# Kernel tuning notes

Measured on AMD Instinct MI355X. Metric: run time of the kernel, lower is better.

Reference implementation:

```python
import jax, jax.numpy as jnp
import numpy as np

QD, KD, HID, NH = 256, 320, 256, 8
NQ, NK, NB = 4096, 4096, 16
DH = HID // NH
EPS = 1e-5
SCALE = float(1.0 / np.sqrt(DH))


def setup_inputs() -> dict:
    key = jax.random.key(0)
    ks = jax.random.split(key, 12)
    s = 0.02
    return {
        "query_nodes": jax.random.normal(ks[0], (NQ, QD), jnp.float32),
        "key_nodes": jax.random.normal(ks[1], (NK, KD), jnp.float32),
        "Wq": jax.random.normal(ks[2], (QD, HID), jnp.float32) * s,
        "bq": jnp.zeros((HID,), jnp.float32),
        "Wk": jax.random.normal(ks[3], (KD, HID), jnp.float32) * s,
        "bk": jnp.zeros((HID,), jnp.float32),
        "Wv": jax.random.normal(ks[4], (KD, HID), jnp.float32) * s,
        "bv": jnp.zeros((HID,), jnp.float32),
        "in_proj_w": jax.random.normal(ks[5], (3 * HID, HID), jnp.float32) * s,
        "in_proj_b": jnp.zeros((3 * HID,), jnp.float32),
        "mha_ow": jax.random.normal(ks[6], (HID, HID), jnp.float32) * s,
        "mha_ob": jnp.zeros((HID,), jnp.float32),
        "Wo": jax.random.normal(ks[7], (HID, QD), jnp.float32) * s,
        "bo": jnp.zeros((QD,), jnp.float32),
        "ln_g": jnp.ones((QD,), jnp.float32),
        "ln_b": jnp.zeros((QD,), jnp.float32),
        "query_batch_idx": jnp.sort(jax.random.randint(ks[8], (NQ,), 0, NB, jnp.int32)),
        "key_batch_idx": jnp.sort(jax.random.randint(ks[9], (NK,), 0, NB, jnp.int32)),
    }


def reference(query_nodes, key_nodes, Wq, bq, Wk, bk, Wv, bv, in_proj_w, in_proj_b,
              mha_ow, mha_ob, Wo, bo, ln_g, ln_b, query_batch_idx, key_batch_idx):
    # outer projections
    q = query_nodes @ Wq + bq          # [NQ, HID]
    k = key_nodes @ Wk + bk            # [NK, HID]
    v = key_nodes @ Wv + bv            # [NK, HID]
    # nn.MultiheadAttention internal in_proj (weights stored [3H, H], applied as x @ W.T)
    q2 = q @ in_proj_w[:HID].T + in_proj_b[:HID]
    k2 = k @ in_proj_w[HID:2 * HID].T + in_proj_b[HID:2 * HID]
    v2 = v @ in_proj_w[2 * HID:].T + in_proj_b[2 * HID:]
    qh = q2.reshape(NQ, NH, DH)
    kh = k2.reshape(NK, NH, DH)
    vh = v2.reshape(NK, NH, DH)
    scores = jnp.einsum('qhd,khd->hqk', qh, kh) * SCALE   # [NH, NQ, NK]
    mask = query_batch_idx[:, None] != key_batch_idx[None, :]  # True = disallowed
    scores = jnp.where(mask[None], -jnp.inf, scores)
    attn = jax.nn.softmax(scores, axis=-1)
    ctx = jnp.einsum('hqk,khd->qhd', attn, vh).reshape(NQ, HID)
    ctx = ctx @ mha_ow + mha_ob        # MHA internal out_proj
    out = ctx @ Wo + bo                # module out_proj back to query_dim
    x = query_nodes + out              # residual (dropout is identity in eval)
    mu = jnp.mean(x, axis=-1, keepdims=True)
    var = jnp.mean((x - mu) ** 2, axis=-1, keepdims=True)
    return (x - mu) / jnp.sqrt(var + EPS) * ln_g + ln_b
```

## Files before the change

kernel.cpp:

```cpp
#include <hip/hip_runtime.h>
#include <hip/hip_bf16.h>
#include <math.h>

#define NQ 4096
#define NK 4096
#define QD 256
#define KD 320
#define HID 256
#define NH 8
#define DH 32
#define NB 16
#define LN_EPS 1e-5f
#define ATT_SCALE 0.17677669529663687f

typedef unsigned short ushort_t;
typedef __attribute__((ext_vector_type(8))) short bf16x8_t;
typedef __attribute__((ext_vector_type(4))) short bf16x4_t;
typedef __attribute__((ext_vector_type(4))) float f32x4_t;

#define OFF_QNB   0
#define OFF_KNB   524288
#define OFF_Q2B   1179648
#define OFF_K2B   1703936
#define OFF_V2B   2228224
#define OFF_CTXB  2752512
#define OFF_XRES  3276800
#define OFF_WQB   4325376
#define OFF_WKB   4358144
#define OFF_WVB   4399104
#define OFF_WINB  4440064
#define OFF_MOWB  4538368
#define OFF_WOTB  4571136
#define OFF_WQT   4603904
#define OFF_WKT   4636672
#define OFF_WVT   4677632
#define OFF_WOT   4718592
#define OFF_BQ    4751360
#define OFF_BK    4751616
#define OFF_BV    4751872
#define OFF_BINP  4752128
#define OFF_MOB   4752896
#define OFF_BO    4753152
#define OFF_LNG   4753408
#define OFF_LNB   4753664
#define OFF_BEFFQ 4753920
#define OFF_BEFFK 4754176
#define OFF_BEFFV 4754432
#define OFF_BEFFO 4754688
#define OFF_KST   4754944
#define OFF_KEN   4754960
#define OFF_FLAG  4754976

__device__ __forceinline__ float bf16_bits_to_f(ushort_t s) {
    unsigned int u = (unsigned int)s << 16;
    float f;
    __builtin_memcpy(&f, &u, 4);
    return f;
}

__device__ __forceinline__ ushort_t f_to_bf16_bits(float v) {
    __hip_bfloat16 t = (__hip_bfloat16)v;
    ushort_t b;
    __builtin_memcpy(&b, &t, 2);
    return b;
}

__global__ void k_detect(const ushort_t* __restrict__ probe,
                         int* __restrict__ flag) {
    __shared__ float red[4];
    int t = threadIdx.x;
    float mx = 0.f;
    for (int i = t; i < 4096; i += 256) {
        float f = fabsf(bf16_bits_to_f(probe[i]));
        if (!(f == f)) f = 1e38f;
        mx = fmaxf(mx, f);
    }
    for (int off = 32; off; off >>= 1) mx = fmaxf(mx, __shfl_xor(mx, off, 64));
    if ((t & 63) == 0) red[t >> 6] = mx;
    __syncthreads();
    if (t == 0) {
        mx = fmaxf(fmaxf(red[0], red[1]), fmaxf(red[2], red[3]));
        *flag = (mx < 100.f) ? 1 : 0;
    }
}

struct Ptrs16 { const void* p[16]; };

#define CVT_TOTAL 2918912

__global__ void k_cvt_all(Ptrs16 ps, float* __restrict__ ws,
                          const int* __restrict__ flag) {
    const int ns[16]   = {1048576,1310720,65536,256,81920,256,81920,256,
                          196608,768,65536,256,65536,256,256,256};
    const int doff[16] = {OFF_QNB,OFF_KNB,OFF_WQB,OFF_BQ,OFF_WKB,OFF_BK,
                          OFF_WVB,OFF_BV,OFF_WINB,OFF_BINP,OFF_MOWB,
                          OFF_MOB,OFF_WOTB,OFF_BO,OFF_LNG,OFF_LNB};
    const int typ[16]  = {0,0,0,1,0,1,0,1,0,1,0,1,2,1,1,1};
    int gid = blockIdx.x * 256 + threadIdx.x;
    if (gid >= CVT_TOTAL) return;
    int fl = *flag;
    int base = 0;
#pragma unroll
    for (int s = 0; s < 16; ++s) {
        int n = ns[s];
        if (gid < base + n) {
            int i = gid - base;
            if (typ[s] == 1) {
                float v = fl ? bf16_bits_to_f(((const ushort_t*)ps.p[s])[i])
                             : ((const float*)ps.p[s])[i];
                ws[doff[s] + i] = v;
            } else {
                ushort_t h = fl ? ((const ushort_t*)ps.p[s])[i]
                                : f_to_bf16_bits(((const float*)ps.p[s])[i]);
                ushort_t* d = (ushort_t*)(ws + doff[s]);
                int di = (typ[s] == 2) ? ((i & 255) * 256 + (i >> 8)) : i;
                d[di] = h;
            }
            return;
        }
        base += n;
    }
}

__global__ void k_ranges(const int* __restrict__ kb, int* __restrict__ kstart,
                         int* __restrict__ kend) {
    int j = blockIdx.x * 256 + threadIdx.x;
    if (j >= NK) return;
    int b = kb[j];
    if (j == 0) {
        for (int x = 0; x < b; ++x) { kstart[x] = 0; kend[x] = 0; }
        kstart[b] = 0;
    } else {
        int bp = kb[j - 1];
        if (bp != b) {
            kend[bp] = j;
            for (int x = bp + 1; x < b; ++x) { kstart[x] = j; kend[x] = j; }
            kstart[b] = j;
        }
    }
    if (j == NK - 1) {
        kend[b] = NK;
        for (int x = b + 1; x < NB; ++x) { kstart[x] = NK; kend[x] = NK; }
    }
}

template <int K>
__device__ __forceinline__ void mm64(const ushort_t* __restrict__ Xrow,
                                     const ushort_t* __restrict__ Wrow,
                                     f32x4_t acc[4]) {
#pragma unroll
    for (int kc = 0; kc < K; kc += 32) {
        bf16x8_t af = *(const bf16x8_t*)(Xrow + kc);
#pragma unroll
        for (int t = 0; t < 4; ++t) {
            bf16x8_t bfrag = *(const bf16x8_t*)(Wrow + t * 16 * K + kc);
            acc[t] = __builtin_amdgcn_mfma_f32_16x16x32_bf16(af, bfrag, acc[t],
                                                             0, 0, 0);
        }
    }
}

__global__ __launch_bounds__(256) void k_fuse_gemm(
        const ushort_t* __restrict__ winb, const ushort_t* __restrict__ wqb,
        const ushort_t* __restrict__ wkb, const ushort_t* __restrict__ wvb,
        const ushort_t* __restrict__ wotb, const ushort_t* __restrict__ mowb,
        ushort_t* __restrict__ wqt, ushort_t* __restrict__ wkt,
        ushort_t* __restrict__ wvt, ushort_t* __restrict__ wot) {
    int r = blockIdx.x;
    const ushort_t *A, *B;
    ushort_t* Out;
    int N, mb, nb;
    if (r < 16)      { A = winb;          B = wqb;  Out = wqt; N = 256; mb = r >> 2;  nb = r & 3; }
    else if (r < 36) { int rr = r - 16; A = winb + 65536;  B = wkb;  Out = wkt; N = 320; mb = rr / 5; nb = rr % 5; }
    else if (r < 56) { int rr = r - 36; A = winb + 131072; B = wvb;  Out = wvt; N = 320; mb = rr / 5; nb = rr % 5; }
    else             { int rr = r - 56; A = wotb;          B = mowb; Out = wot; N = 256; mb = rr >> 2; nb = rr & 3; }
    int w = threadIdx.x >> 6, lane = threadIdx.x & 63;
    int col = lane & 15, quad = lane >> 4;
    int m0 = mb * 64 + w * 16, n0 = nb * 64;
    f32x4_t acc[4];
#pragma unroll
    for (int t = 0; t < 4; ++t) acc[t] = (f32x4_t){0.f, 0.f, 0.f, 0.f};
    mm64<256>(A + (size_t)(m0 + col) * 256 + quad * 8,
              B + (size_t)(n0 + col) * 256 + quad * 8, acc);
#pragma unroll
    for (int t = 0; t < 4; ++t)
#pragma unroll
        for (int rr = 0; rr < 4; ++rr) {
            int m = m0 + quad * 4 + rr;
            int n = n0 + t * 16 + col;
            Out[(size_t)m * N + n] = f_to_bf16_bits(acc[t][rr]);
        }
}

__global__ void k_bias(const float* __restrict__ bq, const float* __restrict__ bk,
                       const float* __restrict__ bv, const float* __restrict__ binp,
                       const float* __restrict__ mob, const float* __restrict__ bo,
                       const ushort_t* __restrict__ winb,
                       const ushort_t* __restrict__ wotb,
                       float* __restrict__ beffQ, float* __restrict__ beffK,
                       float* __restrict__ beffV, float* __restrict__ beffO) {
    int m = blockIdx.x, j = threadIdx.x;
    float acc = 0.f;
    if (m < 3) {
        const float* b = (m == 0) ? bq : (m == 1) ? bk : bv;
        const ushort_t* wrow = winb + (size_t)(m * 256 + j) * 256;
        for (int k = 0; k < 256; ++k) acc += b[k] * bf16_bits_to_f(wrow[k]);
        acc += binp[m * 256 + j];
        float* o = (m == 0) ? beffQ : (m == 1) ? beffK : beffV;
        o[j] = acc;
    } else {
        const ushort_t* wrow = wotb + (size_t)j * 256;
        for (int k = 0; k < 256; ++k) acc += mob[k] * bf16_bits_to_f(wrow[k]);
        acc += bo[j];
        beffO[j] = acc;
    }
}

template <int K, int OUTBF, int RES>
__global__ __launch_bounds__(256) void k_gemm(
        const ushort_t* __restrict__ X,
        const ushort_t* __restrict__ WT0, const ushort_t* __restrict__ WT1,
        const float* __restrict__ b0, const float* __restrict__ b1,
        void* __restrict__ Z0, void* __restrict__ Z1,
        const ushort_t* __restrict__ res) {
    const ushort_t* WT = blockIdx.z ? WT1 : WT0;
    const float* bias  = blockIdx.z ? b1 : b0;
    void* Z            = blockIdx.z ? Z1 : Z0;
    int w = threadIdx.x >> 6, lane = threadIdx.x & 63;
    int col = lane & 15, quad = lane >> 4;
    int m0 = blockIdx.x * 64 + w * 16, n0 = blockIdx.y * 64;
    f32x4_t acc[4];
#pragma unroll
    for (int t = 0; t < 4; ++t) acc[t] = (f32x4_t){0.f, 0.f, 0.f, 0.f};
    mm64<K>(X + (size_t)(m0 + col) * K + quad * 8,
            WT + (size_t)(n0 + col) * K + quad * 8, acc);
#pragma unroll
    for (int t = 0; t < 4; ++t)
#pragma unroll
        for (int rr = 0; rr < 4; ++rr) {
            int m = m0 + quad * 4 + rr;
            int n = n0 + t * 16 + col;
            float v = acc[t][rr] + bias[n];
            if (RES) v += bf16_bits_to_f(res[(size_t)m * 256 + n]);
            size_t idx = (size_t)m * 256 + n;
            if (OUTBF) ((ushort_t*)Z)[idx] = f_to_bf16_bits(v);
            else       ((float*)Z)[idx] = v;
        }
}

__global__ __launch_bounds__(256) void k_attn_mfma(
        const ushort_t* __restrict__ q2b, const ushort_t* __restrict__ k2b,
        const ushort_t* __restrict__ v2b, const int* __restrict__ qb,
        const int* __restrict__ kst, const int* __restrict__ ken,
        ushort_t* __restrict__ ctxb) {
    int wave = threadIdx.x >> 6;
    int lane = threadIdx.x & 63;
    int qt = blockIdx.x >> 1;
    int h  = ((blockIdx.x & 1) << 2) | wave;
    int q0 = qt * 16;
    int col  = lane & 15;
    int quad = lane >> 4;

    int qq = q0 + col;
    int bq_ = qb[qq];
    int j0q = kst[bq_], j1q = ken[bq_];
    int jlo = j0q, jhi = j1q;
#pragma unroll
    for (int off = 1; off < 16; off <<= 1) {
        jlo = min(jlo, __shfl_xor(jlo, off, 64));
        jhi = max(jhi, __shfl_xor(jhi, off, 64));
    }

    bf16x8_t qf = *(const bf16x8_t*)(q2b + (size_t)qq * HID + h * DH + quad * 8);

    f32x4_t accO = {0.f, 0.f, 0.f, 0.f};
    float m_st = -1e30f, l_st = 0.f;

    for (int kt = jlo; kt < jhi; kt += 16) {
        int krow = kt + col;
        if (krow > NK - 1) krow = NK - 1;
        bf16x8_t kf = *(const bf16x8_t*)(k2b + (size_t)krow * HID + h * DH + quad * 8);
        ushort_t vr[4];
#pragma unroll
        for (int j = 0; j < 4; ++j) {
            int vrow = kt + quad * 4 + j;
            if (vrow > NK - 1) vrow = NK - 1;
            vr[j] = v2b[(size_t)vrow * HID + h * DH + col];
        }
        f32x4_t S = __builtin_amdgcn_mfma_f32_16x16x32_bf16(
            kf, qf, (f32x4_t){0.f, 0.f, 0.f, 0.f}, 0, 0, 0);

        float s[4];
        float mt = -3e38f;
#pragma unroll
        for (int r = 0; r < 4; ++r) {
            int kk = kt + quad * 4 + r;
            bool ok = (kk >= j0q) && (kk < j1q);
            s[r] = ok ? S[r] * ATT_SCALE : -3e38f;
            mt = fmaxf(mt, s[r]);
        }
        mt = fmaxf(mt, __shfl_xor(mt, 16, 64));
        mt = fmaxf(mt, __shfl_xor(mt, 32, 64));
        float m_new = fmaxf(m_st, mt);
        float alpha = __expf(m_st - m_new);
        float p[4], ps = 0.f;
#pragma unroll
        for (int r = 0; r < 4; ++r) { p[r] = __expf(s[r] - m_new); ps += p[r]; }
        ps += __shfl_xor(ps, 16, 64);
        ps += __shfl_xor(ps, 32, 64);
        l_st = l_st * alpha + ps;
        m_st = m_new;

        bf16x4_t pb, vb;
#pragma unroll
        for (int r = 0; r < 4; ++r) {
            pb[r] = (short)f_to_bf16_bits(p[r]);
            vb[r] = (short)vr[r];
        }
#pragma unroll
        for (int r = 0; r < 4; ++r) {
            float aq = __shfl(alpha, quad * 4 + r, 64);
            accO[r] *= aq;
        }
        accO = __builtin_amdgcn_mfma_f32_16x16x16bf16_1k(pb, vb, accO, 0, 0, 0);
    }

#pragma unroll
    for (int r = 0; r < 4; ++r) {
        float lq = __shfl(l_st, quad * 4 + r, 64);
        float o = (lq > 0.f) ? accO[r] / lq : 0.f;
        int qrow = q0 + quad * 4 + r;
        ctxb[(size_t)qrow * HID + h * DH + col] = f_to_bf16_bits(o);
    }
}

__global__ void k_ln(const float* __restrict__ X, const float* __restrict__ g,
                     const float* __restrict__ bb, void* __restrict__ out,
                     const int* __restrict__ flag) {
    __shared__ float red[8];
    int q = blockIdx.x, t = threadIdx.x;
    float x = X[(size_t)q * QD + t];
    float s = x, ss = x * x;
    for (int off = 32; off; off >>= 1) {
        s += __shfl_xor(s, off, 64);
        ss += __shfl_xor(ss, off, 64);
    }
    int w = t >> 6;
    if ((t & 63) == 0) { red[w] = s; red[4 + w] = ss; }
    __syncthreads();
    s = red[0] + red[1] + red[2] + red[3];
    ss = red[4] + red[5] + red[6] + red[7];
    float mu = s * (1.f / QD);
    float var = ss * (1.f / QD) - mu * mu;
    float inv = rsqrtf(var + LN_EPS);
    float y = (x - mu) * inv * g[t] + bb[t];
    size_t idx = (size_t)q * QD + t;
    if (*flag)
        ((__hip_bfloat16*)out)[idx] = (__hip_bfloat16)y;
    else
        ((float*)out)[idx] = y;
}

extern "C" void kernel_launch(void* const* d_in, const int* in_sizes, int n_in,
                              void* d_out, int out_size, void* d_ws, size_t ws_size,
                              hipStream_t stream) {
    const int* qbi = (const int*)d_in[16];
    const int* kbi = (const int*)d_in[17];

    float* w = (float*)d_ws;
    ushort_t* qnb  = (ushort_t*)(w + OFF_QNB);
    ushort_t* knb  = (ushort_t*)(w + OFF_KNB);
    ushort_t* q2b  = (ushort_t*)(w + OFF_Q2B);
    ushort_t* k2b  = (ushort_t*)(w + OFF_K2B);
    ushort_t* v2b  = (ushort_t*)(w + OFF_V2B);
    ushort_t* ctxb = (ushort_t*)(w + OFF_CTXB);
    float*    xres = w + OFF_XRES;
    ushort_t* wqb  = (ushort_t*)(w + OFF_WQB);
    ushort_t* wkb  = (ushort_t*)(w + OFF_WKB);
    ushort_t* wvb  = (ushort_t*)(w + OFF_WVB);
    ushort_t* winb = (ushort_t*)(w + OFF_WINB);
    ushort_t* mowb = (ushort_t*)(w + OFF_MOWB);
    ushort_t* wotb = (ushort_t*)(w + OFF_WOTB);
    ushort_t* wqt  = (ushort_t*)(w + OFF_WQT);
    ushort_t* wkt  = (ushort_t*)(w + OFF_WKT);
    ushort_t* wvt  = (ushort_t*)(w + OFF_WVT);
    ushort_t* wot  = (ushort_t*)(w + OFF_WOT);
    float* beffQ = w + OFF_BEFFQ;
    float* beffK = w + OFF_BEFFK;
    float* beffV = w + OFF_BEFFV;
    float* beffO = w + OFF_BEFFO;
    int* kst  = (int*)(w + OFF_KST);
    int* ken  = (int*)(w + OFF_KEN);
    int* flag = (int*)(w + OFF_FLAG);

    Ptrs16 ps;
    for (int i = 0; i < 16; ++i) ps.p[i] = d_in[i];

    k_detect<<<1, 256, 0, stream>>>((const ushort_t*)d_in[0], flag);
    k_cvt_all<<<(CVT_TOTAL + 255) / 256, 256, 0, stream>>>(ps, w, flag);
    k_ranges<<<NK / 256, 256, 0, stream>>>(kbi, kst, ken);
    k_fuse_gemm<<<72, 256, 0, stream>>>(winb, wqb, wkb, wvb, wotb, mowb,
                                        wqt, wkt, wvt, wot);
    k_bias<<<4, 256, 0, stream>>>(w + OFF_BQ, w + OFF_BK, w + OFF_BV,
                                  w + OFF_BINP, w + OFF_MOB, w + OFF_BO,
                                  winb, wotb, beffQ, beffK, beffV, beffO);
    k_gemm<256, 1, 0><<<dim3(NQ / 64, 4, 1), 256, 0, stream>>>(
        qnb, wqt, wqt, beffQ, beffQ, q2b, q2b, nullptr);
    k_gemm<320, 1, 0><<<dim3(NK / 64, 4, 2), 256, 0, stream>>>(
        knb, wkt, wvt, beffK, beffV, k2b, v2b, nullptr);
    k_attn_mfma<<<(NQ / 16) * 2, 256, 0, stream>>>(q2b, k2b, v2b, qbi, kst, ken,
                                                   ctxb);
    k_gemm<256, 0, 1><<<dim3(NQ / 64, 4, 1), 256, 0, stream>>>(
        ctxb, wot, wot, beffO, beffO, xres, xres, qnb);
    k_ln<<<NQ, 256, 0, stream>>>(xres, w + OFF_LNG, w + OFF_LNB, d_out, flag);
}
```

Before: 170.5 us.

## Collapse pipeline into four kernels with on-the-fly conversion and fused out-proj+LayerNorm

Removes the separate detect, convert-all, ranges, weight-fuse and bias kernels by folding detection, key-range computation, weight folding and bias folding into one k_fuse launch. The projections now read the raw inputs directly and convert fp32 to bf16 at load time, which drops the bf16 staging copies. The output projection, residual add and LayerNorm are fused into one kernel where each wave holds a full 256-wide row tile. In exchange, the final kernel runs only 64 blocks with 16 accumulators per lane, which lowers parallelism and adds register pressure, and every block of k_fuse repeats the flag detection.

```diff
diff --git a/kernel.cpp b/kernel.cpp
--- a/kernel.cpp
+++ b/kernel.cpp
@@ -17,39 +17,26 @@
 typedef __attribute__((ext_vector_type(8))) short bf16x8_t;
 typedef __attribute__((ext_vector_type(4))) short bf16x4_t;
 typedef __attribute__((ext_vector_type(4))) float f32x4_t;
-
-#define OFF_QNB   0
-#define OFF_KNB   524288
-#define OFF_Q2B   1179648
-#define OFF_K2B   1703936
-#define OFF_V2B   2228224
-#define OFF_CTXB  2752512
-#define OFF_XRES  3276800
-#define OFF_WQB   4325376
-#define OFF_WKB   4358144
-#define OFF_WVB   4399104
-#define OFF_WINB  4440064
-#define OFF_MOWB  4538368
-#define OFF_WOTB  4571136
-#define OFF_WQT   4603904
-#define OFF_WKT   4636672
-#define OFF_WVT   4677632
-#define OFF_WOT   4718592
-#define OFF_BQ    4751360
-#define OFF_BK    4751616
-#define OFF_BV    4751872
-#define OFF_BINP  4752128
-#define OFF_MOB   4752896
-#define OFF_BO    4753152
-#define OFF_LNG   4753408
-#define OFF_LNB   4753664
-#define OFF_BEFFQ 4753920
-#define OFF_BEFFK 4754176
-#define OFF_BEFFV 4754432
-#define OFF_BEFFO 4754688
-#define OFF_KST   4754944
-#define OFF_KEN   4754960
-#define OFF_FLAG  4754976
+typedef __attribute__((ext_vector_type(8))) unsigned short ushortx8_t;
+
+#define OFF_Q2B   0
+#define OFF_K2B   524288
+#define OFF_V2B   1048576
+#define OFF_CTXB  1572864
+#define OFF_WQT   2097152
+#define OFF_WKT   2129920
+#define OFF_WVT   2170880
+#define OFF_WOT   2211840
+#define OFF_BEFF  2244608
+#define OFF_KST   2245632
+#define OFF_KEN   2245648
+#define OFF_FLAG  2245664
+
+struct KArgs {
+    const void* in[18];
+    float* ws;
+    void* out;
+};
 
 __device__ __forceinline__ float bf16_bits_to_f(ushort_t s) {
     unsigned int u = (unsigned int)s << 16;
@@ -65,194 +52,257 @@
     return b;
 }
 
-__global__ void k_detect(const ushort_t* __restrict__ probe,
-                         int* __restrict__ flag) {
-    __shared__ float red[4];
-    int t = threadIdx.x;
+template <bool F32>
+__device__ __forceinline__ bf16x8_t ld8(const void* p, size_t idx) {
+    if constexpr (!F32) {
+        return *(const bf16x8_t*)((const ushort_t*)p + idx);
+    } else {
+        f32x4_t f0 = *(const f32x4_t*)((const float*)p + idx);
+        f32x4_t f1 = *(const f32x4_t*)((const float*)p + idx + 4);
+        bf16x8_t h;
+#pragma unroll
+        for (int e = 0; e < 4; ++e) h[e] = (short)f_to_bf16_bits(f0[e]);
+#pragma unroll
+        for (int e = 0; e < 4; ++e) h[4 + e] = (short)f_to_bf16_bits(f1[e]);
+        return h;
+    }
+}
+
+template <bool F32>
+__device__ __forceinline__ float ld1f(const void* p, size_t idx) {
+    if constexpr (F32) return ((const float*)p)[idx];
+    else               return bf16_bits_to_f(((const ushort_t*)p)[idx]);
+}
+
+template <bool F32>
+__device__ __forceinline__ ushort_t ld1h(const void* p, size_t idx) {
+    if constexpr (F32) return f_to_bf16_bits(((const float*)p)[idx]);
+    else               return ((const ushort_t*)p)[idx];
+}
+
+__device__ __forceinline__ int detect_flag(const void* probe_v, int tid) {
+    __shared__ float s_red[4];
+    const ushort_t* probe = (const ushort_t*)probe_v;
     float mx = 0.f;
-    for (int i = t; i < 4096; i += 256) {
+    for (int i = tid; i < 4096; i += 256) {
         float f = fabsf(bf16_bits_to_f(probe[i]));
         if (!(f == f)) f = 1e38f;
         mx = fmaxf(mx, f);
     }
     for (int off = 32; off; off >>= 1) mx = fmaxf(mx, __shfl_xor(mx, off, 64));
-    if ((t & 63) == 0) red[t >> 6] = mx;
+    if ((tid & 63) == 0) s_red[tid >> 6] = mx;
     __syncthreads();
-    if (t == 0) {
-        mx = fmaxf(fmaxf(red[0], red[1]), fmaxf(red[2], red[3]));
-        *flag = (mx < 100.f) ? 1 : 0;
-    }
-}
-
-struct Ptrs16 { const void* p[16]; };
-
-#define CVT_TOTAL 2918912
-
-__global__ void k_cvt_all(Ptrs16 ps, float* __restrict__ ws,
-                          const int* __restrict__ flag) {
-    const int ns[16]   = {1048576,1310720,65536,256,81920,256,81920,256,
-                          196608,768,65536,256,65536,256,256,256};
-    const int doff[16] = {OFF_QNB,OFF_KNB,OFF_WQB,OFF_BQ,OFF_WKB,OFF_BK,
-                          OFF_WVB,OFF_BV,OFF_WINB,OFF_BINP,OFF_MOWB,
-                          OFF_MOB,OFF_WOTB,OFF_BO,OFF_LNG,OFF_LNB};
-    const int typ[16]  = {0,0,0,1,0,1,0,1,0,1,0,1,2,1,1,1};
-    int gid = blockIdx.x * 256 + threadIdx.x;
-    if (gid >= CVT_TOTAL) return;
-    int fl = *flag;
-    int base = 0;
-#pragma unroll
-    for (int s = 0; s < 16; ++s) {
-        int n = ns[s];
-        if (gid < base + n) {
-            int i = gid - base;
-            if (typ[s] == 1) {
-                float v = fl ? bf16_bits_to_f(((const ushort_t*)ps.p[s])[i])
-                             : ((const float*)ps.p[s])[i];
-                ws[doff[s] + i] = v;
+    float m2 = fmaxf(fmaxf(s_red[0], s_red[1]), fmaxf(s_red[2], s_red[3]));
+    return (m2 < 100.f) ? 1 : 0;
+}
+
+template <bool F32>
+__device__ __forceinline__ void fuse_qkv_tile(const void* A, size_t abase,
+                                              const void* B, ushort_t* Out,
+                                              int N, int m0, int n0,
+                                              int col, int quad) {
+    f32x4_t acc[4];
+#pragma unroll
+    for (int t = 0; t < 4; ++t) acc[t] = (f32x4_t){0.f, 0.f, 0.f, 0.f};
+    size_t aoff = abase + (size_t)(m0 + col) * 256 + quad * 8;
+    size_t boff = (size_t)(n0 + col) * 256 + quad * 8;
+#pragma unroll
+    for (int kc = 0; kc < 256; kc += 32) {
+        bf16x8_t af = ld8<F32>(A, aoff + kc);
+#pragma unroll
+        for (int t = 0; t < 4; ++t) {
+            bf16x8_t bf = ld8<F32>(B, boff + (size_t)t * 16 * 256 + kc);
+            acc[t] = __builtin_amdgcn_mfma_f32_16x16x32_bf16(af, bf, acc[t], 0, 0, 0);
+        }
+    }
+#pragma unroll
+    for (int t = 0; t < 4; ++t)
+#pragma unroll
+        for (int rr = 0; rr < 4; ++rr)
+            Out[(size_t)(m0 + quad * 4 + rr) * N + n0 + t * 16 + col] =
+                f_to_bf16_bits(acc[t][rr]);
+}
+
+template <bool F32>
+__device__ __forceinline__ void fuse_o_tile(const void* Wo, const void* Mow,
+                                            ushort_t* Out, int m0, int n0,
+                                            int col, int quad) {
+    f32x4_t acc[4];
+#pragma unroll
+    for (int t = 0; t < 4; ++t) acc[t] = (f32x4_t){0.f, 0.f, 0.f, 0.f};
+#pragma unroll
+    for (int kc = 0; kc < 256; kc += 32) {
+        bf16x8_t af;
+#pragma unroll
+        for (int t = 0; t < 8; ++t)
+            af[t] = (short)ld1h<F32>(Wo, (size_t)(kc + quad * 8 + t) * 256 + m0 + col);
+#pragma unroll
+        for (int t = 0; t < 4; ++t) {
+            bf16x8_t bf = ld8<F32>(Mow, (size_t)(n0 + t * 16 + col) * 256 + quad * 8 + kc);
+            acc[t] = __builtin_amdgcn_mfma_f32_16x16x32_bf16(af, bf, acc[t], 0, 0, 0);
+        }
+    }
+#pragma unroll
+    for (int t = 0; t < 4; ++t)
+#pragma unroll
+        for (int rr = 0; rr < 4; ++rr)
+            Out[(size_t)(m0 + quad * 4 + rr) * 256 + n0 + t * 16 + col] =
+                f_to_bf16_bits(acc[t][rr]);
+}
+
+template <bool F32>
+__device__ __forceinline__ void bias_body(KArgs& a, float* ws, int m, int tid) {
+    __shared__ float bsh[256];
+    float* beff = ws + OFF_BEFF;
+    if (m < 3) {
+        const void* bsrc = (m == 0) ? a.in[3] : (m == 1) ? a.in[5] : a.in[7];
+        bsh[tid] = ld1f<F32>(bsrc, tid);
+        __syncthreads();
+        float acc = 0.f;
+        size_t row = (size_t)(m * 256 + tid) * 256;
+#pragma unroll 4
+        for (int kc = 0; kc < 256; kc += 8) {
+            bf16x8_t wr = ld8<F32>(a.in[8], row + kc);
+#pragma unroll
+            for (int t = 0; t < 8; ++t)
+                acc += bsh[kc + t] * bf16_bits_to_f((ushort_t)wr[t]);
+        }
+        acc += ld1f<F32>(a.in[9], m * 256 + tid);
+        beff[m * 256 + tid] = acc;
+    } else {
+        bsh[tid] = ld1f<F32>(a.in[11], tid);
+        __syncthreads();
+        float acc = 0.f;
+        for (int k = 0; k < 256; ++k)
+            acc += bsh[k] * ld1f<F32>(a.in[12], (size_t)k * 256 + tid);
+        acc += ld1f<F32>(a.in[13], tid);
+        beff[3 * 256 + tid] = acc;
+    }
+}
+
+__global__ __launch_bounds__(256) void k_fuse(KArgs a) {
+    float* ws = a.ws;
+    const int tid = threadIdx.x, bid = blockIdx.x;
+    const int lane = tid & 63, wv = tid >> 6;
+    const int col = lane & 15, quad = lane >> 4;
+    int fl = detect_flag(a.in[0], tid);
+    if (bid == 0 && tid == 0) *(int*)(ws + OFF_FLAG) = fl;
+
+    if (bid < 16) {
+        const int* kb = (const int*)a.in[17];
+        int* kstart = (int*)(ws + OFF_KST);
+        int* kend   = (int*)(ws + OFF_KEN);
+        int j = bid * 256 + tid;
+        if (j < NK) {
+            int b = kb[j];
+            if (j == 0) {
+                for (int x = 0; x < b; ++x) { kstart[x] = 0; kend[x] = 0; }
+                kstart[b] = 0;
             } else {
-                ushort_t h = fl ? ((const ushort_t*)ps.p[s])[i]
-                                : f_to_bf16_bits(((const float*)ps.p[s])[i]);
-                ushort_t* d = (ushort_t*)(ws + doff[s]);
-                int di = (typ[s] == 2) ? ((i & 255) * 256 + (i >> 8)) : i;
-                d[di] = h;
+                int bp = kb[j - 1];
+                if (bp != b) {
+                    kend[bp] = j;
+                    for (int x = bp + 1; x < b; ++x) { kstart[x] = j; kend[x] = j; }
+                    kstart[b] = j;
+                }
             }
-            return;
-        }
-        base += n;
-    }
-}
-
-__global__ void k_ranges(const int* __restrict__ kb, int* __restrict__ kstart,
-                         int* __restrict__ kend) {
-    int j = blockIdx.x * 256 + threadIdx.x;
-    if (j >= NK) return;
-    int b = kb[j];
-    if (j == 0) {
-        for (int x = 0; x < b; ++x) { kstart[x] = 0; kend[x] = 0; }
-        kstart[b] = 0;
+            if (j == NK - 1) {
+                kend[b] = NK;
+                for (int x = b + 1; x < NB; ++x) { kstart[x] = NK; kend[x] = NK; }
+            }
+        }
+    } else if (bid < 88) {
+        int r = bid - 16;
+        const void* A; const void* B; ushort_t* Out;
+        size_t abase; int N, mb, nb, typ;
+        if (r < 16)      { typ = 0; A = a.in[8]; abase = 0;      B = a.in[2]; Out = (ushort_t*)(ws + OFF_WQT); N = 256; mb = r >> 2; nb = r & 3; }
+        else if (r < 36) { typ = 0; int rr = r - 16; A = a.in[8]; abase = 65536;  B = a.in[4]; Out = (ushort_t*)(ws + OFF_WKT); N = 320; mb = rr / 5; nb = rr % 5; }
+        else if (r < 56) { typ = 0; int rr = r - 36; A = a.in[8]; abase = 131072; B = a.in[6]; Out = (ushort_t*)(ws + OFF_WVT); N = 320; mb = rr / 5; nb = rr % 5; }
+        else             { typ = 1; int rr = r - 56; A = a.in[12]; abase = 0; B = a.in[10]; Out = (ushort_t*)(ws + OFF_WOT); N = 256; mb = rr >> 2; nb = rr & 3; }
+        int m0 = mb * 64 + wv * 16, n0 = nb * 64;
+        if (typ == 0) {
+            if (fl) fuse_qkv_tile<false>(A, abase, B, Out, N, m0, n0, col, quad);
+            else    fuse_qkv_tile<true >(A, abase, B, Out, N, m0, n0, col, quad);
+        } else {
+            if (fl) fuse_o_tile<false>(A, B, Out, m0, n0, col, quad);
+            else    fuse_o_tile<true >(A, B, Out, m0, n0, col, quad);
+        }
     } else {
-        int bp = kb[j - 1];
-        if (bp != b) {
-            kend[bp] = j;
-            for (int x = bp + 1; x < b; ++x) { kstart[x] = j; kend[x] = j; }
-            kstart[b] = j;
-        }
-    }
-    if (j == NK - 1) {
-        kend[b] = NK;
-        for (int x = b + 1; x < NB; ++x) { kstart[x] = NK; kend[x] = NK; }
-    }
-}
-
-template <int K>
-__device__ __forceinline__ void mm64(const ushort_t* __restrict__ Xrow,
-                                     const ushort_t* __restrict__ Wrow,
-                                     f32x4_t acc[4]) {
-#pragma unroll
-    for (int kc = 0; kc < K; kc += 32) {
-        bf16x8_t af = *(const bf16x8_t*)(Xrow + kc);
+        int m = bid - 88;
+        if (fl) bias_body<false>(a, ws, m, tid);
+        else    bias_body<true >(a, ws, m, tid);
+    }
+}
+
+template <bool F32, int KK>
+__device__ __forceinline__ void proj_body(const void* X, const ushort_t* WT,
+                                          const float* bias, ushort_t* Z,
+                                          int m0, int n0, int col, int quad) {
+    f32x4_t acc[4];
+#pragma unroll
+    for (int t = 0; t < 4; ++t) acc[t] = (f32x4_t){0.f, 0.f, 0.f, 0.f};
+    size_t aoff = (size_t)(m0 + col) * KK + quad * 8;
+    const ushort_t* Wrow = WT + (size_t)(n0 + col) * KK + quad * 8;
+#pragma unroll
+    for (int kc = 0; kc < KK; kc += 32) {
+        bf16x8_t af = ld8<F32>(X, aoff + kc);
 #pragma unroll
         for (int t = 0; t < 4; ++t) {
-            bf16x8_t bfrag = *(const bf16x8_t*)(Wrow + t * 16 * K + kc);
-            acc[t] = __builtin_amdgcn_mfma_f32_16x16x32_bf16(af, bfrag, acc[t],
-                                                             0, 0, 0);
-        }
-    }
-}
-
-__global__ __launch_bounds__(256) void k_fuse_gemm(
-        const ushort_t* __restrict__ winb, const ushort_t* __restrict__ wqb,
-        const ushort_t* __restrict__ wkb, const ushort_t* __restrict__ wvb,
-        const ushort_t* __restrict__ wotb, const ushort_t* __restrict__ mowb,
-        ushort_t* __restrict__ wqt, ushort_t* __restrict__ wkt,
-        ushort_t* __restrict__ wvt, ushort_t* __restrict__ wot) {
-    int r = blockIdx.x;
-    const ushort_t *A, *B;
-    ushort_t* Out;
-    int N, mb, nb;
-    if (r < 16)      { A = winb;          B = wqb;  Out = wqt; N = 256; mb = r >> 2;  nb = r & 3; }
-    else if (r < 36) { int rr = r - 16; A = winb + 65536;  B = wkb;  Out = wkt; N = 320; mb = rr / 5; nb = rr % 5; }
-    else if (r < 56) { int rr = r - 36; A = winb + 131072; B = wvb;  Out = wvt; N = 320; mb = rr / 5; nb = rr % 5; }
-    else             { int rr = r - 56; A = wotb;          B = mowb; Out = wot; N = 256; mb = rr >> 2; nb = rr & 3; }
-    int w = threadIdx.x >> 6, lane = threadIdx.x & 63;
-    int col = lane & 15, quad = lane >> 4;
-    int m0 = mb * 64 + w * 16, n0 = nb * 64;
-    f32x4_t acc[4];
-#pragma unroll
-    for (int t = 0; t < 4; ++t) acc[t] = (f32x4_t){0.f, 0.f, 0.f, 0.f};
-    mm64<256>(A + (size_t)(m0 + col) * 256 + quad * 8,
-              B + (size_t)(n0 + col) * 256 + quad * 8, acc);
+            bf16x8_t bf = *(const bf16x8_t*)(Wrow + (size_t)t * 16 * KK + kc);
+            acc[t] = __builtin_amdgcn_mfma_f32_16x16x32_bf16(af, bf, acc[t], 0, 0, 0);
+        }
+    }
 #pragma unroll
     for (int t = 0; t < 4; ++t)
 #pragma unroll
         for (int rr = 0; rr < 4; ++rr) {
-            int m = m0 + quad * 4 + rr;
             int n = n0 + t * 16 + col;
-            Out[(size_t)m * N + n] = f_to_bf16_bits(acc[t][rr]);
-        }
-}
-
-__global__ void k_bias(const float* __restrict__ bq, const float* __restrict__ bk,
-                       const float* __restrict__ bv, const float* __restrict__ binp,
-                       const float* __restrict__ mob, const float* __restrict__ bo,
-                       const ushort_t* __restrict__ winb,
-                       const ushort_t* __restrict__ wotb,
-                       float* __restrict__ beffQ, float* __restrict__ beffK,
-                       float* __restrict__ beffV, float* __restrict__ beffO) {
-    int m = blockIdx.x, j = threadIdx.x;
-    float acc = 0.f;
-    if (m < 3) {
-        const float* b = (m == 0) ? bq : (m == 1) ? bk : bv;
-        const ushort_t* wrow = winb + (size_t)(m * 256 + j) * 256;
-        for (int k = 0; k < 256; ++k) acc += b[k] * bf16_bits_to_f(wrow[k]);
-        acc += binp[m * 256 + j];
-        float* o = (m == 0) ? beffQ : (m == 1) ? beffK : beffV;
-        o[j] = acc;
+            Z[(size_t)(m0 + quad * 4 + rr) * 256 + n] =
+                f_to_bf16_bits(acc[t][rr] + bias[n]);
+        }
+}
+
+__global__ __launch_bounds__(256) void k_qkv(KArgs a) {
+    float* ws = a.ws;
+    const int tid = threadIdx.x, u = blockIdx.x;
+    const int lane = tid & 63, wv = tid >> 6;
+    const int col = lane & 15, quad = lane >> 4;
+    const int fl = *(const int*)(ws + OFF_FLAG);
+    const float* beff = ws + OFF_BEFF;
+
+    if (u < 256) {
+        int m0 = (u >> 2) * 64 + wv * 16, n0 = (u & 3) * 64;
+        const ushort_t* WT = (const ushort_t*)(ws + OFF_WQT);
+        ushort_t* Z = (ushort_t*)(ws + OFF_Q2B);
+        if (fl) proj_body<false, 256>(a.in[0], WT, beff, Z, m0, n0, col, quad);
+        else    proj_body<true , 256>(a.in[0], WT, beff, Z, m0, n0, col, quad);
+    } else if (u < 512) {
+        int uu = u - 256;
+        int m0 = (uu >> 2) * 64 + wv * 16, n0 = (uu & 3) * 64;
+        const ushort_t* WT = (const ushort_t*)(ws + OFF_WKT);
+        ushort_t* Z = (ushort_t*)(ws + OFF_K2B);
+        if (fl) proj_body<false, 320>(a.in[1], WT, beff + 256, Z, m0, n0, col, quad);
+        else    proj_body<true , 320>(a.in[1], WT, beff + 256, Z, m0, n0, col, quad);
     } else {
-        const ushort_t* wrow = wotb + (size_t)j * 256;
-        for (int k = 0; k < 256; ++k) acc += mob[k] * bf16_bits_to_f(wrow[k]);
-        acc += bo[j];
-        beffO[j] = acc;
-    }
-}
-
-template <int K, int OUTBF, int RES>
-__global__ __launch_bounds__(256) void k_gemm(
-        const ushort_t* __restrict__ X,
-        const ushort_t* __restrict__ WT0, const ushort_t* __restrict__ WT1,
-        const float* __restrict__ b0, const float* __restrict__ b1,
-        void* __restrict__ Z0, void* __restrict__ Z1,
-        const ushort_t* __restrict__ res) {
-    const ushort_t* WT = blockIdx.z ? WT1 : WT0;
-    const float* bias  = blockIdx.z ? b1 : b0;
-    void* Z            = blockIdx.z ? Z1 : Z0;
-    int w = threadIdx.x >> 6, lane = threadIdx.x & 63;
-    int col = lane & 15, quad = lane >> 4;
-    int m0 = blockIdx.x * 64 + w * 16, n0 = blockIdx.y * 64;
-    f32x4_t acc[4];
-#pragma unroll
-    for (int t = 0; t < 4; ++t) acc[t] = (f32x4_t){0.f, 0.f, 0.f, 0.f};
-    mm64<K>(X + (size_t)(m0 + col) * K + quad * 8,
-            WT + (size_t)(n0 + col) * K + quad * 8, acc);
-#pragma unroll
-    for (int t = 0; t < 4; ++t)
-#pragma unroll
-        for (int rr = 0; rr < 4; ++rr) {
-            int m = m0 + quad * 4 + rr;
-            int n = n0 + t * 16 + col;
-            float v = acc[t][rr] + bias[n];
-            if (RES) v += bf16_bits_to_f(res[(size_t)m * 256 + n]);
-            size_t idx = (size_t)m * 256 + n;
-            if (OUTBF) ((ushort_t*)Z)[idx] = f_to_bf16_bits(v);
-            else       ((float*)Z)[idx] = v;
-        }
-}
-
-__global__ __launch_bounds__(256) void k_attn_mfma(
-        const ushort_t* __restrict__ q2b, const ushort_t* __restrict__ k2b,
-        const ushort_t* __restrict__ v2b, const int* __restrict__ qb,
-        const int* __restrict__ kst, const int* __restrict__ ken,
-        ushort_t* __restrict__ ctxb) {
+        int uu = u - 512;
+        int m0 = (uu >> 2) * 64 + wv * 16, n0 = (uu & 3) * 64;
+        const ushort_t* WT = (const ushort_t*)(ws + OFF_WVT);
+        ushort_t* Z = (ushort_t*)(ws + OFF_V2B);
+        if (fl) proj_body<false, 320>(a.in[1], WT, beff + 512, Z, m0, n0, col, quad);
+        else    proj_body<true , 320>(a.in[1], WT, beff + 512, Z, m0, n0, col, quad);
+    }
+}
+
+__global__ __launch_bounds__(256) void k_attn(KArgs a) {
+    float* ws = a.ws;
+    const ushort_t* q2b = (const ushort_t*)(ws + OFF_Q2B);
+    const ushort_t* k2b = (const ushort_t*)(ws + OFF_K2B);
+    const ushort_t* v2b = (const ushort_t*)(ws + OFF_V2B);
+    const int* qb  = (const int*)a.in[16];
+    const int* kst = (const int*)(ws + OFF_KST);
+    const int* ken = (const int*)(ws + OFF_KEN);
+    ushort_t* ctxb = (ushort_t*)(ws + OFF_CTXB);
+
     int wave = threadIdx.x >> 6;
     int lane = threadIdx.x & 63;
     int qt = blockIdx.x >> 1;
@@ -334,83 +384,93 @@
     }
 }
 
-__global__ void k_ln(const float* __restrict__ X, const float* __restrict__ g,
-                     const float* __restrict__ bb, void* __restrict__ out,
-                     const int* __restrict__ flag) {
-    __shared__ float red[8];
-    int q = blockIdx.x, t = threadIdx.x;
-    float x = X[(size_t)q * QD + t];
-    float s = x, ss = x * x;
-    for (int off = 32; off; off >>= 1) {
-        s += __shfl_xor(s, off, 64);
-        ss += __shfl_xor(ss, off, 64);
-    }
-    int w = t >> 6;
-    if ((t & 63) == 0) { red[w] = s; red[4 + w] = ss; }
-    __syncthreads();
-    s = red[0] + red[1] + red[2] + red[3];
-    ss = red[4] + red[5] + red[6] + red[7];
-    float mu = s * (1.f / QD);
-    float var = ss * (1.f / QD) - mu * mu;
-    float inv = rsqrtf(var + LN_EPS);
-    float y = (x - mu) * inv * g[t] + bb[t];
-    size_t idx = (size_t)q * QD + t;
-    if (*flag)
-        ((__hip_bfloat16*)out)[idx] = (__hip_bfloat16)y;
-    else
-        ((float*)out)[idx] = y;
+template <bool F32>
+__device__ __forceinline__ void oln_body(KArgs& a, float* ws, int u,
+                                         int wv, int col, int quad, int fl) {
+    const ushort_t* ctxb = (const ushort_t*)(ws + OFF_CTXB);
+    const ushort_t* wot  = (const ushort_t*)(ws + OFF_WOT);
+    const float* beffO = ws + OFF_BEFF + 3 * 256;
+
+    int m0 = u * 64 + wv * 16;
+    f32x4_t acc[16];
+#pragma unroll
+    for (int t = 0; t < 16; ++t) acc[t] = (f32x4_t){0.f, 0.f, 0.f, 0.f};
+    const ushort_t* Xrow = ctxb + (size_t)(m0 + col) * 256 + quad * 8;
+    const ushort_t* Wbase = wot + (size_t)col * 256 + quad * 8;
+#pragma unroll
+    for (int kc = 0; kc < 256; kc += 32) {
+        bf16x8_t af = *(const bf16x8_t*)(Xrow + kc);
+#pragma unroll
+        for (int t = 0; t < 16; ++t) {
+            bf16x8_t bf = *(const bf16x8_t*)(Wbase + (size_t)t * 16 * 256 + kc);
+            acc[t] = __builtin_amdgcn_mfma_f32_16x16x32_bf16(af, bf, acc[t], 0, 0, 0);
+        }
+    }
+    float s_[4] = {0.f, 0.f, 0.f, 0.f};
+    float ss_[4] = {0.f, 0.f, 0.f, 0.f};
+#pragma unroll
+    for (int t = 0; t < 16; ++t) {
+        int n = t * 16 + col;
+        float b = beffO[n];
+#pragma unroll
+        for (int rr = 0; rr < 4; ++rr) {
+            int m = m0 + quad * 4 + rr;
+            float x = acc[t][rr] + b + ld1f<F32>(a.in[0], (size_t)m * 256 + n);
+            acc[t][rr] = x;
+            s_[rr] += x;
+            ss_[rr] += x * x;
+        }
+    }
+#pragma unroll
+    for (int off = 1; off < 16; off <<= 1) {
+#pragma unroll
+        for (int rr = 0; rr < 4; ++rr) {
+            s_[rr]  += __shfl_xor(s_[rr],  off, 16);
+            ss_[rr] += __shfl_xor(ss_[rr], off, 16);
+        }
+    }
+    float mu[4], inv[4];
+#pragma unroll
+    for (int rr = 0; rr < 4; ++rr) {
+        mu[rr] = s_[rr] * (1.f / QD);
+        float var = ss_[rr] * (1.f / QD) - mu[rr] * mu[rr];
+        inv[rr] = rsqrtf(var + LN_EPS);
+    }
+#pragma unroll
+    for (int t = 0; t < 16; ++t) {
+        int n = t * 16 + col;
+        float g = ld1f<F32>(a.in[14], n), bb = ld1f<F32>(a.in[15], n);
+#pragma unroll
+        for (int rr = 0; rr < 4; ++rr) {
+            int m = m0 + quad * 4 + rr;
+            float y = (acc[t][rr] - mu[rr]) * inv[rr] * g + bb;
+            size_t idx = (size_t)m * 256 + n;
+            if (fl) ((ushort_t*)a.out)[idx] = f_to_bf16_bits(y);
+            else    ((float*)a.out)[idx] = y;
+        }
+    }
+}
+
+__global__ __launch_bounds__(256) void k_oln(KArgs a) {
+    float* ws = a.ws;
+    const int tid = threadIdx.x;
+    const int lane = tid & 63, wv = tid >> 6;
+    const int col = lane & 15, quad = lane >> 4;
+    const int fl = *(const int*)(ws + OFF_FLAG);
+    if (fl) oln_body<false>(a, ws, blockIdx.x, wv, col, quad, fl);
+    else    oln_body<true >(a, ws, blockIdx.x, wv, col, quad, fl);
 }
 
 extern "C" void kernel_launch(void* const* d_in, const int* in_sizes, int n_in,
                               void* d_out, int out_size, void* d_ws, size_t ws_size,
                               hipStream_t stream) {
-    const int* qbi = (const int*)d_in[16];
-    const int* kbi = (const int*)d_in[17];
-
-    float* w = (float*)d_ws;
-    ushort_t* qnb  = (ushort_t*)(w + OFF_QNB);
-    ushort_t* knb  = (ushort_t*)(w + OFF_KNB);
-    ushort_t* q2b  = (ushort_t*)(w + OFF_Q2B);
-    ushort_t* k2b  = (ushort_t*)(w + OFF_K2B);
-    ushort_t* v2b  = (ushort_t*)(w + OFF_V2B);
-    ushort_t* ctxb = (ushort_t*)(w + OFF_CTXB);
-    float*    xres = w + OFF_XRES;
-    ushort_t* wqb  = (ushort_t*)(w + OFF_WQB);
-    ushort_t* wkb  = (ushort_t*)(w + OFF_WKB);
-    ushort_t* wvb  = (ushort_t*)(w + OFF_WVB);
-    ushort_t* winb = (ushort_t*)(w + OFF_WINB);
-    ushort_t* mowb = (ushort_t*)(w + OFF_MOWB);
-    ushort_t* wotb = (ushort_t*)(w + OFF_WOTB);
-    ushort_t* wqt  = (ushort_t*)(w + OFF_WQT);
-    ushort_t* wkt  = (ushort_t*)(w + OFF_WKT);
-    ushort_t* wvt  = (ushort_t*)(w + OFF_WVT);
-    ushort_t* wot  = (ushort_t*)(w + OFF_WOT);
-    float* beffQ = w + OFF_BEFFQ;
-    float* beffK = w + OFF_BEFFK;
-    float* beffV = w + OFF_BEFFV;
-    float* beffO = w + OFF_BEFFO;
-    int* kst  = (int*)(w + OFF_KST);
-    int* ken  = (int*)(w + OFF_KEN);
-    int* flag = (int*)(w + OFF_FLAG);
-
-    Ptrs16 ps;
-    for (int i = 0; i < 16; ++i) ps.p[i] = d_in[i];
-
-    k_detect<<<1, 256, 0, stream>>>((const ushort_t*)d_in[0], flag);
-    k_cvt_all<<<(CVT_TOTAL + 255) / 256, 256, 0, stream>>>(ps, w, flag);
-    k_ranges<<<NK / 256, 256, 0, stream>>>(kbi, kst, ken);
-    k_fuse_gemm<<<72, 256, 0, stream>>>(winb, wqb, wkb, wvb, wotb, mowb,
-                                        wqt, wkt, wvt, wot);
-    k_bias<<<4, 256, 0, stream>>>(w + OFF_BQ, w + OFF_BK, w + OFF_BV,
-                                  w + OFF_BINP, w + OFF_MOB, w + OFF_BO,
-                                  winb, wotb, beffQ, beffK, beffV, beffO);
-    k_gemm<256, 1, 0><<<dim3(NQ / 64, 4, 1), 256, 0, stream>>>(
-        qnb, wqt, wqt, beffQ, beffQ, q2b, q2b, nullptr);
-    k_gemm<320, 1, 0><<<dim3(NK / 64, 4, 2), 256, 0, stream>>>(
-        knb, wkt, wvt, beffK, beffV, k2b, v2b, nullptr);
-    k_attn_mfma<<<(NQ / 16) * 2, 256, 0, stream>>>(q2b, k2b, v2b, qbi, kst, ken,
-                                                   ctxb);
-    k_gemm<256, 0, 1><<<dim3(NQ / 64, 4, 1), 256, 0, stream>>>(
-        ctxb, wot, wot, beffO, beffO, xres, xres, qnb);
-    k_ln<<<NQ, 256, 0, stream>>>(xres, w + OFF_LNG, w + OFF_LNB, d_out, flag);
-}
+    KArgs a;
+    for (int i = 0; i < 18; ++i) a.in[i] = d_in[i];
+    a.ws = (float*)d_ws;
+    a.out = d_out;
+
+    k_fuse<<<92, 256, 0, stream>>>(a);
+    k_qkv<<<768, 256, 0, stream>>>(a);
+    k_attn<<<512, 256, 0, stream>>>(a);
+    k_oln<<<64, 256, 0, stream>>>(a);
+}
```

After: 166.8 us. -2.2%, faster.
